# Kernel tuning notes

Measured on AMD Instinct MI355X. Metric: run time of the kernel, lower is better.

Reference implementation:

```python
import jax, jax.numpy as jnp
import numpy as np

D_MODEL = 1024
NUM_HEADS = 16
SCALE = 1.0 / np.sqrt(D_MODEL // NUM_HEADS)  # matches sqrt(d_model // num_heads)


def setup_inputs() -> dict:
    key = jax.random.key(0)
    ks = jax.random.split(key, 7)
    B, S, D = 4, 2048, D_MODEL
    std = 1.0 / np.sqrt(D)
    return {
        "x": jax.random.normal(ks[0], (B, S, D), dtype=jnp.float32),
        "Wq": jax.random.normal(ks[1], (D, D), dtype=jnp.float32) * std,
        "bq": jnp.zeros((D,), dtype=jnp.float32),
        "Wk": jax.random.normal(ks[2], (D, D), dtype=jnp.float32) * std,
        "bk": jnp.zeros((D,), dtype=jnp.float32),
        "Wv": jax.random.normal(ks[3], (D, D), dtype=jnp.float32) * std,
        "bv": jnp.zeros((D,), dtype=jnp.float32),
    }


def reference(x, Wq, bq, Wk, bk, Wv, bv):
    # QKV projections (nn.Linear: x @ W^T + b; here W stored as [in, out] already)
    Q = x @ Wq + bq  # [B, S, D]
    K = x @ Wk + bk
    V = x @ Wv + bv
    scores = jnp.einsum("bsd,btd->bst", Q, K) * SCALE  # [B, S, S]
    S_len = x.shape[1]
    causal = jnp.tril(jnp.ones((S_len, S_len), dtype=bool))
    scores = jnp.where(causal, scores, -jnp.inf)
    attn = jax.nn.softmax(scores, axis=-1)
    return jnp.einsum("bst,btd->bsd", attn, V)
```

## Files before the change

kernel.cpp:

```cpp
#include <hip/hip_runtime.h>
#include <hip/hip_bf16.h>
#include <cstdint>

#define D_MODEL 1024
#define SEQ     2048
#define SCALE   0.125f
#define P_ELEMS 2228224

typedef __attribute__((ext_vector_type(8))) _Float16 f16x8;
typedef __attribute__((ext_vector_type(8))) unsigned short u16x8;
typedef __attribute__((ext_vector_type(4))) float f32x4;

__device__ __forceinline__ unsigned short f2h(float f) {
  _Float16 h = (_Float16)f;
  return __builtin_bit_cast(unsigned short, h);
}
__device__ __forceinline__ float h2f(unsigned short u) {
  return (float)__builtin_bit_cast(_Float16, u);
}

__device__ __forceinline__ void gll16(const void* g, void* lds_p) {
  __builtin_amdgcn_global_load_lds(
      (const __attribute__((address_space(1))) unsigned int*)(uintptr_t)g,
      (__attribute__((address_space(3))) unsigned int*)(unsigned int)(uintptr_t)lds_p,
      16, 0, 0);
}

#define WAITV8 asm volatile("s_waitcnt vmcnt(8)" ::: "memory")
#define WAITV0 asm volatile("s_waitcnt vmcnt(0)" ::: "memory")
#define WAITL8 asm volatile("s_waitcnt lgkmcnt(8)" ::: "memory")
#define WAITL0 asm volatile("s_waitcnt lgkmcnt(0)" ::: "memory")
#define SCHEDB __builtin_amdgcn_sched_barrier(0)
#define BAR    __builtin_amdgcn_s_barrier()
#define PRIO1  __builtin_amdgcn_s_setprio(1)
#define PRIO0  __builtin_amdgcn_s_setprio(0)
#define MFMA16(a, b, c) __builtin_amdgcn_mfma_f32_16x16x32_f16(a, b, c, 0, 0, 0)

__device__ __forceinline__ void stage_tile(const unsigned short* gA, const unsigned short* gB,
                                           size_t sA, size_t sB,
                                           int k0, unsigned short* buf, int w, int lane) {
  int rl = lane >> 3;
  int sg = ((lane & 7) ^ rl) << 3;
#pragma unroll
  for (int j = 0; j < 4; j++) {
    int c = w * 4 + j;
    int row = c * 8 + rl;
    gll16(gA + (size_t)row * sA + k0 + sg, buf + c * 512);
    gll16(gB + (size_t)row * sB + k0 + sg, buf + 8192 + c * 512);
  }
}

__device__ __forceinline__ void gemm_core(const unsigned short* gA, const unsigned short* gB,
                                          size_t sA, size_t sB,
                                          unsigned short* lds0, unsigned short* lds1, int nt,
                                          int w, int lane, int wr, int wc, int l15, int l4,
                                          f32x4 acc[4][4]) {
  stage_tile(gA, gB, sA, sB, 0, lds0, w, lane);
  stage_tile(gA, gB, sA, sB, 64, lds1, w, lane);
  WAITV8; SCHEDB; BAR;
  for (int t = 0; t < nt; t++) {
    const unsigned short* buf = (t & 1) ? lds1 : lds0;
    const unsigned short* bA = buf;
    const unsigned short* bB = buf + 8192;
    f16x8 a0[4], b0[4], a1[4], b1[4];
#pragma unroll
    for (int m = 0; m < 4; m++) {
      int row = wr * 64 + m * 16 + l15, rs = row & 7;
      a0[m] = *(const f16x8*)(bA + row * 64 + ((l4 ^ rs) << 3));
    }
#pragma unroll
    for (int n = 0; n < 4; n++) {
      int row = wc * 64 + n * 16 + l15, rs = row & 7;
      b0[n] = *(const f16x8*)(bB + row * 64 + ((l4 ^ rs) << 3));
    }
#pragma unroll
    for (int m = 0; m < 4; m++) {
      int row = wr * 64 + m * 16 + l15, rs = row & 7;
      a1[m] = *(const f16x8*)(bA + row * 64 + (((4 + l4) ^ rs) << 3));
    }
#pragma unroll
    for (int n = 0; n < 4; n++) {
      int row = wc * 64 + n * 16 + l15, rs = row & 7;
      b1[n] = *(const f16x8*)(bB + row * 64 + (((4 + l4) ^ rs) << 3));
    }
    WAITL8; SCHEDB;
    PRIO1;
#pragma unroll
    for (int m = 0; m < 4; m++)
#pragma unroll
      for (int n = 0; n < 4; n++)
        acc[m][n] = MFMA16(a0[m], b0[n], acc[m][n]);
    PRIO0;
    WAITL0; SCHEDB; BAR;
    if (t + 2 < nt) stage_tile(gA, gB, sA, sB, (t + 2) * 64,
                               (unsigned short*)buf, w, lane);
    PRIO1;
#pragma unroll
    for (int m = 0; m < 4; m++)
#pragma unroll
      for (int n = 0; n < 4; n++)
        acc[m][n] = MFMA16(a1[m], b1[n], acc[m][n]);
    PRIO0;
    if (t + 2 < nt) { WAITV8; } else { WAITV0; }
    SCHEDB; BAR;
  }
}

__global__ __launch_bounds__(256) void cvt_fused(const float* __restrict__ x,
                                                 const float* __restrict__ W0,
                                                 const float* __restrict__ W1,
                                                 const float* __restrict__ W2,
                                                 unsigned short* __restrict__ xb,
                                                 unsigned short* __restrict__ wt) {
  __shared__ float t[32][33];
  int bid = blockIdx.x;
  int tid = threadIdx.x;
  if (bid < 4096) {
    int i = bid * 256 + tid;
    const float4* p = (const float4*)x + (size_t)i * 2;
    float4 a = p[0], b = p[1];
    u16x8 r;
    r[0] = f2h(a.x); r[1] = f2h(a.y); r[2] = f2h(a.z); r[3] = f2h(a.w);
    r[4] = f2h(b.x); r[5] = f2h(b.y); r[6] = f2h(b.z); r[7] = f2h(b.w);
    *((u16x8*)xb + i) = r;
  } else {
    int id = bid - 4096;
    int z = id >> 10, rem = id & 1023;
    int bx = rem & 31, by = rem >> 5;
    const float* W = (z == 0) ? W0 : (z == 1 ? W1 : W2);
    unsigned short* o = wt + (size_t)z * 1048576;
    int c0 = bx * 32, r0 = by * 32;
    int tx = tid & 31, ty = tid >> 5;
    for (int i = 0; i < 4; i++)
      t[ty + 8 * i][tx] = W[(size_t)(r0 + ty + 8 * i) * 1024 + c0 + tx];
    __syncthreads();
    for (int i = 0; i < 4; i++)
      o[(size_t)(c0 + ty + 8 * i) * 1024 + r0 + tx] = f2h(t[tx][ty + 8 * i]);
  }
}

__global__ __launch_bounds__(256) void qkv_gemm(const unsigned short* __restrict__ xb,
                                                const unsigned short* __restrict__ wt,
                                                const float* __restrict__ b0,
                                                const float* __restrict__ b1,
                                                const float* __restrict__ b2,
                                                unsigned short* __restrict__ Qp,
                                                unsigned short* __restrict__ Kp,
                                                unsigned short* __restrict__ vtp) {
  __shared__ unsigned short lds[2][16384];
  int m0 = blockIdx.x * 128;
  int n0 = blockIdx.y * 128;
  int z = n0 >> 10, nz = n0 & 1023;
  const unsigned short* gA = xb + (size_t)m0 * 1024;
  const unsigned short* gB = wt + (size_t)z * 1048576 + (size_t)nz * 1024;
  const float* bias = (z == 0) ? b0 : (z == 1 ? b1 : b2);
  int tid = threadIdx.x, lane = tid & 63, w = tid >> 6;
  int wr = w >> 1, wc = w & 1, l15 = lane & 15, l4 = lane >> 4;
  f32x4 acc[4][4] = {};
  gemm_core(gA, gB, 1024, 1024, &lds[0][0], &lds[1][0], 16, w, lane, wr, wc, l15, l4, acc);

  if (z < 2) {
    unsigned short* O = (z == 0) ? Qp : Kp;
#pragma unroll
    for (int m = 0; m < 4; m++)
#pragma unroll
      for (int n = 0; n < 4; n++) {
        int cl = wc * 64 + n * 16 + l15;
        float bv = bias[nz + cl];
#pragma unroll
        for (int r = 0; r < 4; r++) {
          int row = m0 + wr * 64 + m * 16 + l4 * 4 + r;
          O[(size_t)row * 1024 + nz + cl] = f2h(acc[m][n][r] + bv);
        }
      }
  } else {
    unsigned short* T = &lds[0][0];
#pragma unroll
    for (int m = 0; m < 4; m++)
#pragma unroll
      for (int n = 0; n < 4; n++) {
        int cl = wc * 64 + n * 16 + l15;
        float bv = bias[nz + cl];
#pragma unroll
        for (int r = 0; r < 4; r++) {
          int rl = wr * 64 + m * 16 + l4 * 4 + r;
          T[cl * 136 + rl] = f2h(acc[m][n][r] + bv);
        }
      }
    __syncthreads();
    int bidx = m0 >> 11, s0 = m0 & 2047;
#pragma unroll
    for (int i = 0; i < 8; i++) {
      int d = w * 32 + i * 4 + (lane >> 4);
      int ch = lane & 15;
      u16x8 v = *(const u16x8*)(T + d * 136 + ch * 8);
      *(u16x8*)(vtp + ((size_t)bidx * 1024 + nz + d) * 2048 + s0 + ch * 8) = v;
    }
  }
}

__global__ __launch_bounds__(256) void qk_scores(const unsigned short* __restrict__ Q,
                                                 const unsigned short* __restrict__ Kb,
                                                 unsigned short* __restrict__ sc) {
  __shared__ unsigned short lds[2][16384];
  int blk = blockIdx.x;
  int t0, ntile;
  if (blk < 32) { t0 = 480 + blk; ntile = 2; }
  else          { t0 = blk - 32;  ntile = 1; }
  int tid = threadIdx.x, lane = tid & 63, w = tid >> 6;
  int wr = w >> 1, wc = w & 1, l15 = lane & 15, l4 = lane >> 4;
  for (int u = 0; u < ntile; u++) {
    int ti = t0 + u * 32;
    int b = ti / 136, i = ti % 136;
    int qt = (int)((sqrtf(8.f * i + 1.f) - 1.f) * 0.5f);
    while ((qt + 1) * (qt + 2) / 2 <= i) qt++;
    while (qt * (qt + 1) / 2 > i) qt--;
    int kt = i - qt * (qt + 1) / 2;
    int Wspan = (qt + 1) << 7;
    const unsigned short* gA = Q  + ((size_t)b * 2048 + qt * 128) * 1024;
    const unsigned short* gB = Kb + ((size_t)b * 2048 + kt * 128) * 1024;
    unsigned short* outp = sc + (size_t)b * P_ELEMS + (size_t)16384 * (qt * (qt + 1) / 2);
    f32x4 acc[4][4] = {};
    gemm_core(gA, gB, 1024, 1024, &lds[0][0], &lds[1][0], 16, w, lane, wr, wc, l15, l4, acc);
#pragma unroll
    for (int m = 0; m < 4; m++)
#pragma unroll
      for (int n = 0; n < 4; n++) {
        int cl = wc * 64 + n * 16 + l15;
        int kv = kt * 128 + cl;
#pragma unroll
        for (int r = 0; r < 4; r++) {
          int rl = wr * 64 + m * 16 + l4 * 4 + r;
          int srow = qt * 128 + rl;
          float v = acc[m][n][r] * SCALE;
          if (kv > srow) v = -30000.f;
          outp[(size_t)rl * Wspan + kv] = f2h(v);
        }
      }
  }
}

__global__ __launch_bounds__(256) void softmax_row(const unsigned short* __restrict__ sc,
                                                   unsigned short* __restrict__ pb) {
  __shared__ float redm[4];
  __shared__ float reds[4];
  int srow = blockIdx.x;
  int b = srow >> 11, sl = srow & 2047;
  int qt = sl >> 7;
  int Wspan = (qt + 1) << 7;
  size_t rb = (size_t)b * P_ELEMS + (size_t)16384 * (qt * (qt + 1) / 2) + (size_t)(sl & 127) * Wspan;
  const u16x8* src = (const u16x8*)(sc + rb);
  int nv = Wspan >> 3;
  int t = threadIdx.x, lane = t & 63, w = t >> 6;
  bool h0 = t < nv;
  float v[8];
  float mx = -1e30f;
  if (h0) {
    u16x8 raw = src[t];
#pragma unroll
    for (int j = 0; j < 8; j++) { v[j] = h2f(raw[j]); mx = fmaxf(mx, v[j]); }
  }
  for (int off = 1; off < 64; off <<= 1) mx = fmaxf(mx, __shfl_xor(mx, off, 64));
  if (lane == 0) redm[w] = mx;
  __syncthreads();
  mx = fmaxf(fmaxf(redm[0], redm[1]), fmaxf(redm[2], redm[3]));
  float s = 0.f;
  if (h0) {
#pragma unroll
    for (int j = 0; j < 8; j++) { v[j] = __expf(v[j] - mx); s += v[j]; }
  }
  for (int off = 1; off < 64; off <<= 1) s += __shfl_xor(s, off, 64);
  if (lane == 0) reds[w] = s;
  __syncthreads();
  s = reds[0] + reds[1] + reds[2] + reds[3];
  float inv = 1.f / s;
  if (h0) {
    u16x8 o;
#pragma unroll
    for (int j = 0; j < 8; j++) o[j] = f2h(v[j] * inv);
    *((u16x8*)(pb + rb) + t) = o;
  }
}

__global__ __launch_bounds__(256) void pv_gemm(const unsigned short* __restrict__ pb,
                                               const unsigned short* __restrict__ vtp,
                                               float* __restrict__ outp) {
  __shared__ unsigned short lds[2][16384];
  int bx = blockIdx.x;
  int n0 = blockIdx.y * 128;
  int bz = blockIdx.z;
  int qt = (bz & 2) ? (15 - bx) : bx;
  int b = bz;
  int tid = threadIdx.x, lane = tid & 63, w = tid >> 6;
  int wr = w >> 1, wc = w & 1, l15 = lane & 15, l4 = lane >> 4;
  const unsigned short* gB = vtp + (size_t)b * 1024 * 2048 + (size_t)n0 * 2048;
  int Wspan = (qt + 1) << 7;
  const unsigned short* gA = pb + (size_t)b * P_ELEMS + (size_t)16384 * (qt * (qt + 1) / 2);
  float* O = outp + ((size_t)b * 2048 + qt * 128) * 1024;
  f32x4 acc[4][4] = {};
  gemm_core(gA, gB, Wspan, 2048, &lds[0][0], &lds[1][0], 2 * (qt + 1),
            w, lane, wr, wc, l15, l4, acc);
#pragma unroll
  for (int m = 0; m < 4; m++)
#pragma unroll
    for (int n = 0; n < 4; n++) {
      int cl = n0 + wc * 64 + n * 16 + l15;
#pragma unroll
      for (int r = 0; r < 4; r++) {
        int rl = wr * 64 + m * 16 + l4 * 4 + r;
        O[(size_t)rl * 1024 + cl] = acc[m][n][r];
      }
    }
}

extern "C" void kernel_launch(void* const* d_in, const int* in_sizes, int n_in,
                              void* d_out, int out_size, void* d_ws, size_t ws_size,
                              hipStream_t stream) {
  const float* x  = (const float*)d_in[0];
  const float* Wq = (const float*)d_in[1];
  const float* bq = (const float*)d_in[2];
  const float* Wk = (const float*)d_in[3];
  const float* bk = (const float*)d_in[4];
  const float* Wv = (const float*)d_in[5];
  const float* bv = (const float*)d_in[6];
  float* out = (float*)d_out;

  unsigned short* ws  = (unsigned short*)d_ws;
  unsigned short* wt  = ws;
  unsigned short* Qp  = ws + 3145728;
  unsigned short* Kp  = ws + 11534336;
  unsigned short* vtp = ws + 19922944;
  unsigned short* sc  = ws + 28311552;
  unsigned short* pb  = ws + 37224448;
  unsigned short* xb  = (unsigned short*)d_out;

  cvt_fused<<<7168, 256, 0, stream>>>(x, Wq, Wk, Wv, xb, wt);
  qkv_gemm<<<dim3(64, 24), 256, 0, stream>>>(xb, wt, bq, bk, bv, Qp, Kp, vtp);
  qk_scores<<<512, 256, 0, stream>>>(Qp, Kp, sc);
  softmax_row<<<8192, 256, 0, stream>>>(sc, pb);
  pv_gemm<<<dim3(16, 8, 4), 256, 0, stream>>>(pb, vtp, out);
}
```

Before: 150.6 us.

## Stage GEMM epilogues through LDS for vector stores; one wave per softmax row

The QKV, QK-score and PV GEMM epilogues now write the tile into shared memory first. They then emit coalesced 16-byte stores instead of scattered 2- or 4-byte stores; the PV path uses an XOR swizzle to avoid bank conflicts. Softmax now processes four rows per block, one wave each, so cross-wave reductions and block barriers are gone. This adds extra barriers and LDS traffic in the epilogues.

```diff
diff --git a/kernel.cpp b/kernel.cpp
--- a/kernel.cpp
+++ b/kernel.cpp
@@ -159,6 +159,7 @@
   f32x4 acc[4][4] = {};
   gemm_core(gA, gB, 1024, 1024, &lds[0][0], &lds[1][0], 16, w, lane, wr, wc, l15, l4, acc);
 
+  unsigned short* T = &lds[0][0];
   if (z < 2) {
     unsigned short* O = (z == 0) ? Qp : Kp;
 #pragma unroll
@@ -169,12 +170,19 @@
         float bv = bias[nz + cl];
 #pragma unroll
         for (int r = 0; r < 4; r++) {
-          int row = m0 + wr * 64 + m * 16 + l4 * 4 + r;
-          O[(size_t)row * 1024 + nz + cl] = f2h(acc[m][n][r] + bv);
+          int rl = wr * 64 + m * 16 + l4 * 4 + r;
+          T[rl * 136 + cl] = f2h(acc[m][n][r] + bv);
         }
       }
+    __syncthreads();
+#pragma unroll
+    for (int i = 0; i < 8; i++) {
+      int idx = i * 256 + tid;
+      int row = idx >> 4, ch = idx & 15;
+      u16x8 v = *(const u16x8*)(T + row * 136 + ch * 8);
+      *(u16x8*)(O + (size_t)(m0 + row) * 1024 + nz + ch * 8) = v;
+    }
   } else {
-    unsigned short* T = &lds[0][0];
 #pragma unroll
     for (int m = 0; m < 4; m++)
 #pragma unroll
@@ -222,6 +230,7 @@
     unsigned short* outp = sc + (size_t)b * P_ELEMS + (size_t)16384 * (qt * (qt + 1) / 2);
     f32x4 acc[4][4] = {};
     gemm_core(gA, gB, 1024, 1024, &lds[0][0], &lds[1][0], 16, w, lane, wr, wc, l15, l4, acc);
+    unsigned short* T = &lds[0][0];
 #pragma unroll
     for (int m = 0; m < 4; m++)
 #pragma unroll
@@ -234,52 +243,80 @@
           int srow = qt * 128 + rl;
           float v = acc[m][n][r] * SCALE;
           if (kv > srow) v = -30000.f;
-          outp[(size_t)rl * Wspan + kv] = f2h(v);
+          T[rl * 136 + cl] = f2h(v);
         }
       }
+    __syncthreads();
+#pragma unroll
+    for (int i2 = 0; i2 < 8; i2++) {
+      int idx = i2 * 256 + tid;
+      int row = idx >> 4, ch = idx & 15;
+      u16x8 v = *(const u16x8*)(T + row * 136 + ch * 8);
+      *(u16x8*)(outp + (size_t)row * Wspan + kt * 128 + ch * 8) = v;
+    }
+    __syncthreads();
   }
 }
 
 __global__ __launch_bounds__(256) void softmax_row(const unsigned short* __restrict__ sc,
                                                    unsigned short* __restrict__ pb) {
-  __shared__ float redm[4];
-  __shared__ float reds[4];
-  int srow = blockIdx.x;
-  int b = srow >> 11, sl = srow & 2047;
+  int base = blockIdx.x * 4;
+  int b = base >> 11, sl0 = base & 2047;
+  int w = threadIdx.x >> 6, lane = threadIdx.x & 63;
+  int sl = sl0 + w;
   int qt = sl >> 7;
   int Wspan = (qt + 1) << 7;
   size_t rb = (size_t)b * P_ELEMS + (size_t)16384 * (qt * (qt + 1) / 2) + (size_t)(sl & 127) * Wspan;
   const u16x8* src = (const u16x8*)(sc + rb);
-  int nv = Wspan >> 3;
-  int t = threadIdx.x, lane = t & 63, w = t >> 6;
-  bool h0 = t < nv;
-  float v[8];
+  int nc = Wspan >> 3;
+  bool h0 = lane < nc, h1 = lane + 64 < nc, h2 = lane + 128 < nc, h3 = lane + 192 < nc;
+  float v0[8], v1[8], v2[8], v3[8];
   float mx = -1e30f;
-  if (h0) {
-    u16x8 raw = src[t];
-#pragma unroll
-    for (int j = 0; j < 8; j++) { v[j] = h2f(raw[j]); mx = fmaxf(mx, v[j]); }
-  }
+  if (h0) { u16x8 r = src[lane];
+#pragma unroll
+    for (int j = 0; j < 8; j++) { v0[j] = h2f(r[j]); mx = fmaxf(mx, v0[j]); } }
+  if (h1) { u16x8 r = src[lane + 64];
+#pragma unroll
+    for (int j = 0; j < 8; j++) { v1[j] = h2f(r[j]); mx = fmaxf(mx, v1[j]); } }
+  if (h2) { u16x8 r = src[lane + 128];
+#pragma unroll
+    for (int j = 0; j < 8; j++) { v2[j] = h2f(r[j]); mx = fmaxf(mx, v2[j]); } }
+  if (h3) { u16x8 r = src[lane + 192];
+#pragma unroll
+    for (int j = 0; j < 8; j++) { v3[j] = h2f(r[j]); mx = fmaxf(mx, v3[j]); } }
   for (int off = 1; off < 64; off <<= 1) mx = fmaxf(mx, __shfl_xor(mx, off, 64));
-  if (lane == 0) redm[w] = mx;
-  __syncthreads();
-  mx = fmaxf(fmaxf(redm[0], redm[1]), fmaxf(redm[2], redm[3]));
   float s = 0.f;
   if (h0) {
 #pragma unroll
-    for (int j = 0; j < 8; j++) { v[j] = __expf(v[j] - mx); s += v[j]; }
-  }
+    for (int j = 0; j < 8; j++) { v0[j] = __expf(v0[j] - mx); s += v0[j]; } }
+  if (h1) {
+#pragma unroll
+    for (int j = 0; j < 8; j++) { v1[j] = __expf(v1[j] - mx); s += v1[j]; } }
+  if (h2) {
+#pragma unroll
+    for (int j = 0; j < 8; j++) { v2[j] = __expf(v2[j] - mx); s += v2[j]; } }
+  if (h3) {
+#pragma unroll
+    for (int j = 0; j < 8; j++) { v3[j] = __expf(v3[j] - mx); s += v3[j]; } }
   for (int off = 1; off < 64; off <<= 1) s += __shfl_xor(s, off, 64);
-  if (lane == 0) reds[w] = s;
-  __syncthreads();
-  s = reds[0] + reds[1] + reds[2] + reds[3];
   float inv = 1.f / s;
-  if (h0) {
-    u16x8 o;
-#pragma unroll
-    for (int j = 0; j < 8; j++) o[j] = f2h(v[j] * inv);
-    *((u16x8*)(pb + rb) + t) = o;
-  }
+  u16x8* dst = (u16x8*)(pb + rb);
+  if (h0) { u16x8 o;
+#pragma unroll
+    for (int j = 0; j < 8; j++) o[j] = f2h(v0[j] * inv);
+    dst[lane] = o; }
+  if (h1) { u16x8 o;
+#pragma unroll
+    for (int j = 0; j < 8; j++) o[j] = f2h(v1[j] * inv);
+    dst[lane + 64] = o; }
+  if (h2) { u16x8 o;
+#pragma unroll
+    for (int j = 0; j < 8; j++) o[j] = f2h(v2[j] * inv);
+    dst[lane + 128] = o; }
+  if (h3) { u16x8 o;
+#pragma unroll
+    for (int j = 0; j < 8; j++) o[j] = f2h(v3[j] * inv);
+    dst[lane + 192] = o; }
 }
 
 __global__ __launch_bounds__(256) void pv_gemm(const unsigned short* __restrict__ pb,
@@ -300,17 +337,28 @@
   f32x4 acc[4][4] = {};
   gemm_core(gA, gB, Wspan, 2048, &lds[0][0], &lds[1][0], 2 * (qt + 1),
             w, lane, wr, wc, l15, l4, acc);
+  float* Tf = (float*)&lds[0][0];
 #pragma unroll
   for (int m = 0; m < 4; m++)
 #pragma unroll
     for (int n = 0; n < 4; n++) {
-      int cl = n0 + wc * 64 + n * 16 + l15;
+      int cl = wc * 64 + n * 16 + l15;
 #pragma unroll
       for (int r = 0; r < 4; r++) {
         int rl = wr * 64 + m * 16 + l4 * 4 + r;
-        O[(size_t)rl * 1024 + cl] = acc[m][n][r];
+        int cc = cl >> 2;
+        int sw = (((cc ^ (rl & 7)) << 2) | (cl & 3));
+        Tf[rl * 128 + sw] = acc[m][n][r];
       }
     }
+  __syncthreads();
+#pragma unroll
+  for (int i = 0; i < 16; i++) {
+    int idx = i * 256 + tid;
+    int row = idx >> 5, ch = idx & 31;
+    float4 val = *(const float4*)&Tf[row * 128 + ((ch ^ (row & 7)) << 2)];
+    *(float4*)&O[(size_t)row * 1024 + n0 + ch * 4] = val;
+  }
 }
 
 extern "C" void kernel_launch(void* const* d_in, const int* in_sizes, int n_in,
@@ -337,6 +385,6 @@
   cvt_fused<<<7168, 256, 0, stream>>>(x, Wq, Wk, Wv, xb, wt);
   qkv_gemm<<<dim3(64, 24), 256, 0, stream>>>(xb, wt, bq, bk, bv, Qp, Kp, vtp);
   qk_scores<<<512, 256, 0, stream>>>(Qp, Kp, sc);
-  softmax_row<<<8192, 256, 0, stream>>>(sc, pb);
+  softmax_row<<<2048, 256, 0, stream>>>(sc, pb);
   pv_gemm<<<dim3(16, 8, 4), 256, 0, stream>>>(pb, vtp, out);
 }
```

Result: no change. 149.7 us (-0.6%).
